# Kernel optimization log

Measured on AMD Instinct MI355X. Metric: run time of the kernel, lower is better.

## Reference

```python
import jax, jax.numpy as jnp
import numpy as np

B, S, D = 32, 8192, 64


def setup_inputs() -> dict:
    key = jax.random.key(0)
    k1, k2 = jax.random.split(key)
    input_real = jax.random.normal(k1, (B, S, D), dtype=jnp.float32)
    input_imag = jax.random.normal(k2, (B, S, D), dtype=jnp.float32)
    return {"input_real": input_real, "input_imag": input_imag}


def reference(input_real, input_imag):
    # ComplexMixture: mean over seq of per-token complex outer products v v^H.
    # Original builds [B,S,D,D] via 4 batch_dots then means over S; fused here
    # as Gram contractions over the sequence axis (no [B,S,D,D] intermediate).
    seq_len = input_real.shape[1]
    inv_s = jnp.asarray(1.0 / seq_len, dtype=input_real.dtype)
    rr = jnp.einsum('bsi,bsj->bij', input_real, input_real)
    ii = jnp.einsum('bsi,bsj->bij', input_imag, input_imag)
    ri = jnp.einsum('bsi,bsj->bij', input_real, input_imag)
    out_real = (rr + ii) * inv_s                     # [B, D, D], symmetric
    out_imag = (ri - jnp.swapaxes(ri, 1, 2)) * inv_s  # [B, D, D], antisymmetric
    return (out_real, out_imag)
```

## Files before the change

### kernel.cpp

```cpp
#include <hip/hip_runtime.h>


#define BATCH 32
#define SEQ   8192
#define DD    64
#define BK    128

typedef __bf16 bf16x8 __attribute__((ext_vector_type(8)));
typedef float  f32x16 __attribute__((ext_vector_type(16)));

__device__ __forceinline__ unsigned bf16pk(float a, float b) {
  unsigned ua = __builtin_bit_cast(unsigned, a);
  unsigned ub = __builtin_bit_cast(unsigned, b);
  ua = (ua + 0x7fffu + ((ua >> 16) & 1u)) >> 16;
  ub = (ub + 0x7fffu + ((ub >> 16) & 1u)) >> 16;
  return (ua & 0xffffu) | (ub << 16);
}

template<int CHUNKS>
__global__ __launch_bounds__(256, 4) void gram_partial(
    const float* __restrict__ R, const float* __restrict__ I,
    float* __restrict__ ws)
{
  constexpr int SCHUNK = SEQ / CHUNKS;
  constexpr int NIT    = SCHUNK / BK;
  __shared__ uint4 lds[32][64];
  const int tid  = threadIdx.x;
  const int wave = tid >> 6;
  const int lane = tid & 63;
  const int b = blockIdx.x & 31;
  const int c = blockIdx.x >> 5;
  const float* Rb = R + (size_t)b * (SEQ * DD);
  const float* Ib = I + (size_t)b * (SEQ * DD);
  const int m0 = (wave >> 1) * 32;
  const int n0 = (wave & 1) * 32;
  const int l31 = lane & 31;
  const int lhi = lane >> 5;

  f32x16 accR = {};
  f32x16 accI = {};

  const int chunk0 = c * SCHUNK;

  for (int it = 0; it < NIT; ++it) {
    const int sbase = chunk0 + it * BK;
    float rv[4][8], iv[4][8];
    #pragma unroll
    for (int gi = 0; gi < 4; ++gi) {
      const int g = gi * 4 + wave;
      const float* pR = Rb + (size_t)(sbase + g * 8) * DD + lane;
      const float* pI = Ib + (size_t)(sbase + g * 8) * DD + lane;
      #pragma unroll
      for (int j = 0; j < 8; ++j) { rv[gi][j] = pR[j * 64]; iv[gi][j] = pI[j * 64]; }
    }
    #pragma unroll
    for (int gi = 0; gi < 4; ++gi) {
      const int g = gi * 4 + wave;
      uint4 qR; qR.x = bf16pk(rv[gi][0], rv[gi][1]); qR.y = bf16pk(rv[gi][2], rv[gi][3]);
                qR.z = bf16pk(rv[gi][4], rv[gi][5]); qR.w = bf16pk(rv[gi][6], rv[gi][7]);
      uint4 qI; qI.x = bf16pk(iv[gi][0], iv[gi][1]); qI.y = bf16pk(iv[gi][2], iv[gi][3]);
                qI.z = bf16pk(iv[gi][4], iv[gi][5]); qI.w = bf16pk(iv[gi][6], iv[gi][7]);
      lds[g][lane]      = qR;
      lds[16 + g][lane] = qI;
    }
    __syncthreads();
    #pragma unroll
    for (int ks = 0; ks < BK / 16; ++ks) {
      const int kg = ks * 2 + lhi;
      bf16x8 aR = __builtin_bit_cast(bf16x8, lds[kg][m0 + l31]);
      bf16x8 bR = __builtin_bit_cast(bf16x8, lds[kg][n0 + l31]);
      bf16x8 aI = __builtin_bit_cast(bf16x8, lds[16 + kg][m0 + l31]);
      bf16x8 bI = __builtin_bit_cast(bf16x8, lds[16 + kg][n0 + l31]);
      accR = __builtin_amdgcn_mfma_f32_32x32x16_bf16(aR, bR, accR, 0, 0, 0);
      accR = __builtin_amdgcn_mfma_f32_32x32x16_bf16(aI, bI, accR, 0, 0, 0);
      accI = __builtin_amdgcn_mfma_f32_32x32x16_bf16(aR, bI, accI, 0, 0, 0);
    }
    __syncthreads();
  }

  float* wsR = ws + ((size_t)(c * 32 + b) * 2) * 4096;
  float* wsM = wsR + 4096;
  const int jj = n0 + l31;
  #pragma unroll
  for (int r = 0; r < 16; ++r) {
    const int i = m0 + (r & 3) + 8 * (r >> 2) + 4 * lhi;
    wsR[i * 64 + jj] = accR[r];
  }
  float* ldsf = (float*)lds;
  #pragma unroll
  for (int r = 0; r < 16; ++r) {
    const int i = m0 + (r & 3) + 8 * (r >> 2) + 4 * lhi;
    ldsf[i * 65 + jj] = accI[r];
  }
  __syncthreads();
  #pragma unroll
  for (int k = 0; k < 16; ++k) {
    const int e = tid + 256 * k;
    const int i = e >> 6, j = e & 63;
    wsM[e] = ldsf[i * 65 + j] - ldsf[j * 65 + i];
  }
}

template<int CHUNKS>
__global__ __launch_bounds__(256) void gram_reduce(
    const float4* __restrict__ ws, float4* __restrict__ out)
{
  const int o = blockIdx.x * 256 + threadIdx.x;
  const int kind = o >> 15;
  const int rem  = o & 32767;
  const int b    = rem >> 10;
  const int e    = rem & 1023;
  const float inv = 1.0f / (float)SEQ;
  float sx = 0.f, sy = 0.f, sz = 0.f, sw = 0.f;
  #pragma unroll
  for (int c = 0; c < CHUNKS; ++c) {
    float4 v = ws[((size_t)(c * 32 + b) * 2 + kind) * 1024 + e];
    sx += v.x; sy += v.y; sz += v.z; sw += v.w;
  }
  float4 r; r.x = sx * inv; r.y = sy * inv; r.z = sz * inv; r.w = sw * inv;
  out[o] = r;
}

extern "C" void kernel_launch(void* const* d_in, const int* in_sizes, int n_in,
                              void* d_out, int out_size, void* d_ws, size_t ws_size,
                              hipStream_t stream) {
  const float* R = (const float*)d_in[0];
  const float* I = (const float*)d_in[1];
  float* out = (float*)d_out;
  float* ws  = (float*)d_ws;

  const size_t need32 = (size_t)32 * 32 * 2 * 4096 * 4;
  if (ws_size >= need32) {
    gram_partial<32><<<BATCH * 32, 256, 0, stream>>>(R, I, ws);
    gram_reduce<32><<<256, 256, 0, stream>>>((const float4*)ws, (float4*)out);
  } else {
    gram_partial<16><<<BATCH * 16, 256, 0, stream>>>(R, I, ws);
    gram_reduce<16><<<256, 256, 0, stream>>>((const float4*)ws, (float4*)out);
  }
}
```

Measured before the change: 175.0 us.

## Double-buffer LDS tiles with register prefetch and swizzled vector loads

Adds a two-stage LDS double buffer: the next tile's global loads are issued into registers before the current tile's MFMAs, then packed into the other buffer, so only one barrier is needed per iteration. Global loads become 16-byte vector loads, with a permuted LDS column index to avoid bank conflicts. The default split drops from 32 to 16 chunks per batch, and launch bounds are lowered to 2 blocks per SM. The aim is to hide memory latency and halve barrier and reduction overhead, at the cost of fewer resident blocks and fewer total blocks (512) to cover the memory-bound input read.

Measured after the change: 154.3 us. 1.13x faster.

```diff
diff --git a/kernel.cpp b/kernel.cpp
--- a/kernel.cpp
+++ b/kernel.cpp
@@ -8,6 +8,7 @@
 
 typedef __bf16 bf16x8 __attribute__((ext_vector_type(8)));
 typedef float  f32x16 __attribute__((ext_vector_type(16)));
+typedef float  f32x4  __attribute__((ext_vector_type(4)));
 
 __device__ __forceinline__ unsigned bf16pk(float a, float b) {
   unsigned ua = __builtin_bit_cast(unsigned, a);
@@ -17,14 +18,18 @@
   return (ua & 0xffffu) | (ub << 16);
 }
 
+__device__ __forceinline__ int permd(int d) {
+  return d ^ ((d >> 3) & 1) ^ (((d >> 4) & 1) << 1);
+}
+
 template<int CHUNKS>
-__global__ __launch_bounds__(256, 4) void gram_partial(
+__global__ __launch_bounds__(256, 2) void gram_partial(
     const float* __restrict__ R, const float* __restrict__ I,
     float* __restrict__ ws)
 {
   constexpr int SCHUNK = SEQ / CHUNKS;
   constexpr int NIT    = SCHUNK / BK;
-  __shared__ uint4 lds[32][64];
+  __shared__ uint4 lds[2][32][64];
   const int tid  = threadIdx.x;
   const int wave = tid >> 6;
   const int lane = tid & 63;
@@ -32,51 +37,80 @@
   const int c = blockIdx.x >> 5;
   const float* Rb = R + (size_t)b * (SEQ * DD);
   const float* Ib = I + (size_t)b * (SEQ * DD);
-  const int m0 = (wave >> 1) * 32;
-  const int n0 = (wave & 1) * 32;
+  const int m0  = (wave >> 1) * 32;
+  const int n0  = (wave & 1) * 32;
   const int l31 = lane & 31;
   const int lhi = lane >> 5;
+  const int g   = tid >> 4;
+  const int q   = tid & 15;
+  const int pa  = permd(m0 + l31);
+  const int pb  = permd(n0 + l31);
+  int pw[4];
+  #pragma unroll
+  for (int cc = 0; cc < 4; ++cc) pw[cc] = permd(q * 4 + cc);
 
   f32x16 accR = {};
   f32x16 accI = {};
-
   const int chunk0 = c * SCHUNK;
 
+  f32x4 rv[8], iv[8];
+
+#define LOADT(it_) do { \
+    const size_t sb_ = (size_t)(chunk0 + (it_) * BK + g * 8); \
+    const f32x4* pR_ = (const f32x4*)(Rb + sb_ * DD) + q; \
+    const f32x4* pI_ = (const f32x4*)(Ib + sb_ * DD) + q; \
+    _Pragma("unroll") \
+    for (int j = 0; j < 8; ++j) { rv[j] = pR_[j * 16]; iv[j] = pI_[j * 16]; } \
+    asm volatile("" ::: "memory"); \
+  } while (0)
+
+#define PACKW(buf_) do { \
+    _Pragma("unroll") \
+    for (int cc = 0; cc < 4; ++cc) { \
+      uint4 qR_, qI_; \
+      qR_.x = bf16pk(rv[0][cc], rv[1][cc]); qR_.y = bf16pk(rv[2][cc], rv[3][cc]); \
+      qR_.z = bf16pk(rv[4][cc], rv[5][cc]); qR_.w = bf16pk(rv[6][cc], rv[7][cc]); \
+      qI_.x = bf16pk(iv[0][cc], iv[1][cc]); qI_.y = bf16pk(iv[2][cc], iv[3][cc]); \
+      qI_.z = bf16pk(iv[4][cc], iv[5][cc]); qI_.w = bf16pk(iv[6][cc], iv[7][cc]); \
+      lds[buf_][g][pw[cc]]      = qR_; \
+      lds[buf_][16 + g][pw[cc]] = qI_; \
+    } \
+  } while (0)
+
+#define TILEBAR() do { \
+    __builtin_amdgcn_sched_barrier(0); \
+    asm volatile("s_waitcnt lgkmcnt(0)" ::: "memory"); \
+    __builtin_amdgcn_s_barrier(); \
+    __builtin_amdgcn_sched_barrier(0); \
+  } while (0)
+
+  LOADT(0);
+  PACKW(0);
+  TILEBAR();
+
+  #pragma unroll
   for (int it = 0; it < NIT; ++it) {
-    const int sbase = chunk0 + it * BK;
-    float rv[4][8], iv[4][8];
-    #pragma unroll
-    for (int gi = 0; gi < 4; ++gi) {
-      const int g = gi * 4 + wave;
-      const float* pR = Rb + (size_t)(sbase + g * 8) * DD + lane;
-      const float* pI = Ib + (size_t)(sbase + g * 8) * DD + lane;
-      #pragma unroll
-      for (int j = 0; j < 8; ++j) { rv[gi][j] = pR[j * 64]; iv[gi][j] = pI[j * 64]; }
-    }
-    #pragma unroll
-    for (int gi = 0; gi < 4; ++gi) {
-      const int g = gi * 4 + wave;
-      uint4 qR; qR.x = bf16pk(rv[gi][0], rv[gi][1]); qR.y = bf16pk(rv[gi][2], rv[gi][3]);
-                qR.z = bf16pk(rv[gi][4], rv[gi][5]); qR.w = bf16pk(rv[gi][6], rv[gi][7]);
-      uint4 qI; qI.x = bf16pk(iv[gi][0], iv[gi][1]); qI.y = bf16pk(iv[gi][2], iv[gi][3]);
-                qI.z = bf16pk(iv[gi][4], iv[gi][5]); qI.w = bf16pk(iv[gi][6], iv[gi][7]);
-      lds[g][lane]      = qR;
-      lds[16 + g][lane] = qI;
-    }
-    __syncthreads();
+    const int buf = it & 1;
+    if (it + 1 < NIT) LOADT(it + 1);
     #pragma unroll
     for (int ks = 0; ks < BK / 16; ++ks) {
       const int kg = ks * 2 + lhi;
-      bf16x8 aR = __builtin_bit_cast(bf16x8, lds[kg][m0 + l31]);
-      bf16x8 bR = __builtin_bit_cast(bf16x8, lds[kg][n0 + l31]);
-      bf16x8 aI = __builtin_bit_cast(bf16x8, lds[16 + kg][m0 + l31]);
-      bf16x8 bI = __builtin_bit_cast(bf16x8, lds[16 + kg][n0 + l31]);
+      bf16x8 aR = __builtin_bit_cast(bf16x8, lds[buf][kg][pa]);
+      bf16x8 bR = __builtin_bit_cast(bf16x8, lds[buf][kg][pb]);
+      bf16x8 aI = __builtin_bit_cast(bf16x8, lds[buf][16 + kg][pa]);
+      bf16x8 bI = __builtin_bit_cast(bf16x8, lds[buf][16 + kg][pb]);
       accR = __builtin_amdgcn_mfma_f32_32x32x16_bf16(aR, bR, accR, 0, 0, 0);
       accR = __builtin_amdgcn_mfma_f32_32x32x16_bf16(aI, bI, accR, 0, 0, 0);
       accI = __builtin_amdgcn_mfma_f32_32x32x16_bf16(aR, bI, accI, 0, 0, 0);
     }
-    __syncthreads();
+    if (it + 1 < NIT) {
+      PACKW(buf ^ 1);
+      TILEBAR();
+    }
   }
+#undef LOADT
+#undef PACKW
+#undef TILEBAR
 
   float* wsR = ws + ((size_t)(c * 32 + b) * 2) * 4096;
   float* wsM = wsR + 4096;
@@ -113,8 +147,8 @@
   const float inv = 1.0f / (float)SEQ;
   float sx = 0.f, sy = 0.f, sz = 0.f, sw = 0.f;
   #pragma unroll
-  for (int c = 0; c < CHUNKS; ++c) {
-    float4 v = ws[((size_t)(c * 32 + b) * 2 + kind) * 1024 + e];
+  for (int cc = 0; cc < CHUNKS; ++cc) {
+    float4 v = ws[((size_t)(cc * 32 + b) * 2 + kind) * 1024 + e];
     sx += v.x; sy += v.y; sz += v.z; sw += v.w;
   }
   float4 r; r.x = sx * inv; r.y = sy * inv; r.z = sz * inv; r.w = sw * inv;
@@ -129,12 +163,12 @@
   float* out = (float*)d_out;
   float* ws  = (float*)d_ws;
 
-  const size_t need32 = (size_t)32 * 32 * 2 * 4096 * 4;
-  if (ws_size >= need32) {
-    gram_partial<32><<<BATCH * 32, 256, 0, stream>>>(R, I, ws);
-    gram_reduce<32><<<256, 256, 0, stream>>>((const float4*)ws, (float4*)out);
-  } else {
+  const size_t need16 = (size_t)16 * 32 * 2 * 4096 * 4;
+  if (ws_size >= need16) {
     gram_partial<16><<<BATCH * 16, 256, 0, stream>>>(R, I, ws);
     gram_reduce<16><<<256, 256, 0, stream>>>((const float4*)ws, (float4*)out);
+  } else {
+    gram_partial<8><<<BATCH * 8, 256, 0, stream>>>(R, I, ws);
+    gram_reduce<8><<<256, 256, 0, stream>>>((const float4*)ws, (float4*)out);
   }
 }
```
